# Kernel optimization log

Hardware: AMD Instinct MI355X
Metric: run time of the kernel (lower is better)

The kernel has to match this reference:

```python
import jax, jax.numpy as jnp
import numpy as np

CAPACITY_FACTOR = 1.0


def setup_inputs() -> dict:
    key = jax.random.key(0)
    ks = jax.random.split(key, 6)
    B, S, D, H, E = 4, 2048, 1024, 4096, 8
    scale_in = 1.0 / np.sqrt(D)
    scale_h = 1.0 / np.sqrt(H)
    return {
        "inputs": jax.random.normal(ks[0], (B, S, D), dtype=jnp.float32),
        "router_w": jax.random.normal(ks[1], (E, D), dtype=jnp.float32) * scale_in,
        "w1": jax.random.normal(ks[2], (E, D, H), dtype=jnp.float32) * scale_in,
        "b1": jnp.zeros((E, H), dtype=jnp.float32),
        "w2": jax.random.normal(ks[3], (E, H, D), dtype=jnp.float32) * scale_h,
        "b2": jnp.zeros((E, D), dtype=jnp.float32),
    }


def reference(inputs, router_w, w1, b1, w2, b2):
    B, S, D = inputs.shape
    E = router_w.shape[0]
    x = inputs.reshape(-1, D)                     # [T, D], T = B*S
    T = x.shape[0]
    top_k = int(CAPACITY_FACTOR * T / E)          # static: 1024

    # Router + softmax over experts (softmax_topk order), fp32 like the original
    router_logits = x @ router_w.T                # [T, E]
    all_probs = jax.nn.softmax(router_logits.astype(jnp.float32), axis=-1)

    # Expert-choice: each expert picks its top_k tokens
    weights, selected_tokens = jax.lax.top_k(all_probs.T, top_k)  # [E, K]

    # Gather tokens per expert: [E, K, D]
    xg = x[selected_tokens]

    # Per-expert MLP as grouped GEMMs (Linear -> GELU(exact) -> Linear)
    h = jax.nn.gelu(jnp.einsum("ekd,edh->ekh", xg, w1) + b1[:, None, :],
                    approximate=False)
    out = jnp.einsum("ekh,ehd->ekd", h, w2) + b2[:, None, :]   # [E, K, D]

    # Weighted scatter-add combine (indices unique within an expert;
    # cross-expert duplicates accumulate, matching the per-expert += loop)
    out = out * weights[..., None].astype(out.dtype)
    results = jnp.zeros_like(x).at[selected_tokens.reshape(-1)].add(
        out.reshape(-1, D))

    return results.reshape(B, S, D), router_logits, selected_tokens
```

## Files before the change

kernel.cpp:

```cpp
#include <hip/hip_runtime.h>
#include <hip/hip_bf16.h>
#include <math.h>

#define T_TOK 8192
#define E_EXP 8
#define D_DIM 1024
#define H_DIM 4096
#define K_CAP 1024

typedef __attribute__((ext_vector_type(8))) short short8;
typedef __attribute__((ext_vector_type(4))) float floatx4;
typedef __attribute__((ext_vector_type(16))) float floatx16;

typedef __attribute__((address_space(3))) unsigned int lds_u32_t;
typedef __attribute__((address_space(1))) unsigned int gbl_u32_t;
#define ASYNC_CP16(gptr, lptr) \
  __builtin_amdgcn_global_load_lds((gbl_u32_t*)(gptr), (lds_u32_t*)(lptr), 16, 0, 0)

static __device__ __forceinline__ unsigned int f2bf_u(float f) {
  union { float f; unsigned int u; } v; v.f = f;
  unsigned int r = v.u + 0x7FFF + ((v.u >> 16) & 1);
  return r >> 16;
}

__global__ __launch_bounds__(256) void zero_kernel(float* __restrict__ p, int n4) {
  int i = blockIdx.x * 256 + threadIdx.x;
  if (i < n4) ((floatx4*)p)[i] = (floatx4)0.0f;
}

template <int KD, int ND>
__global__ __launch_bounds__(256)
void transpose_kernel(const float* __restrict__ w, unsigned short* __restrict__ wt) {
  int e = blockIdx.z;
  int n0 = blockIdx.x * 64, k0 = blockIdx.y * 64;
  __shared__ float ts[64][65];
  int tid = threadIdx.x;
  int rr = tid >> 4;
  int cc = (tid & 15) * 4;
  const float* src = w + ((size_t)e * KD + k0 + rr) * ND + n0 + cc;
#pragma unroll
  for (int it = 0; it < 4; it++) {
    float4 v = *(const float4*)(src + (size_t)it * 16 * ND);
    int r = rr + it * 16;
    ts[r][cc + 0] = v.x; ts[r][cc + 1] = v.y; ts[r][cc + 2] = v.z; ts[r][cc + 3] = v.w;
  }
  __syncthreads();
  int n = tid >> 3;
  int k8 = (tid & 7) * 8;
#pragma unroll
  for (int it = 0; it < 2; it++) {
    int nn = n + it * 32;
    unsigned int u[4];
#pragma unroll
    for (int j = 0; j < 4; j++)
      u[j] = f2bf_u(ts[k8 + 2 * j][nn]) | (f2bf_u(ts[k8 + 2 * j + 1][nn]) << 16);
    *(uint4*)&wt[((size_t)e * ND + n0 + nn) * KD + k0 + k8] = *(uint4*)u;
  }
}

__global__ __launch_bounds__(256)
void router_kernel(const float* __restrict__ x, const float* __restrict__ rw,
                   float* __restrict__ logits_out, float* __restrict__ probs_ws,
                   unsigned long long* __restrict__ keys_ws,
                   unsigned short* __restrict__ x_bf) {
  int t = blockIdx.x;
  int tid = threadIdx.x;
  int lane = tid & 63, wid = tid >> 6;
  __shared__ float xs[D_DIM];
  __shared__ double dred[4 * E_EXP];
  __shared__ double dlog[E_EXP];
  for (int i = tid; i < D_DIM; i += 256) xs[i] = x[(size_t)t * D_DIM + i];
  __syncthreads();
  {
    int i4 = tid * 4;
    uint2 u;
    u.x = f2bf_u(xs[i4 + 0]) | (f2bf_u(xs[i4 + 1]) << 16);
    u.y = f2bf_u(xs[i4 + 2]) | (f2bf_u(xs[i4 + 3]) << 16);
    ((uint2*)(x_bf + (size_t)t * D_DIM))[tid] = u;
  }
#pragma unroll
  for (int e = 0; e < E_EXP; e++) {
    double s = 0.0;
#pragma unroll
    for (int i = 0; i < 4; i++) {
      int d = tid + i * 256;
      s += (double)xs[d] * (double)rw[e * D_DIM + d];
    }
#pragma unroll
    for (int off = 32; off > 0; off >>= 1) s += __shfl_down(s, off, 64);
    if (lane == 0) dred[wid * E_EXP + e] = s;
  }
  __syncthreads();
  if (tid < E_EXP) {
    double s = dred[tid] + dred[E_EXP + tid] + dred[2 * E_EXP + tid] + dred[3 * E_EXP + tid];
    dlog[tid] = s;
    logits_out[(size_t)t * E_EXP + tid] = (float)s;
  }
  __syncthreads();
  if (tid == 0) {
    double m = dlog[0];
#pragma unroll
    for (int e = 1; e < E_EXP; e++) m = dlog[e] > m ? dlog[e] : m;
    double ex[E_EXP], Z = 0.0;
#pragma unroll
    for (int e = 0; e < E_EXP; e++) { ex[e] = exp(dlog[e] - m); Z += ex[e]; }
#pragma unroll
    for (int e = 0; e < E_EXP; e++) {
      double p = ex[e] / Z;
      probs_ws[e * T_TOK + t] = (float)p;
      unsigned long long b = (unsigned long long)__double_as_longlong(p);
      keys_ws[e * T_TOK + t] = (b & ~8191ULL) | (unsigned long long)(8191 - t);
    }
  }
}

__global__ __launch_bounds__(256)
void topk_kernel(const unsigned long long* __restrict__ keys_ws,
                 const float* __restrict__ probs_ws,
                 int* __restrict__ sel_ws, float* __restrict__ wt_ws,
                 float* __restrict__ selout) {
  int e = blockIdx.x >> 5, seg = blockIdx.x & 31;
  int tid = threadIdx.x;
  const unsigned long long* keys = keys_ws + (size_t)e * T_TOK;
  __shared__ unsigned long long kbuf[2048];
  int t = seg * 256 + tid;
  unsigned long long own = keys[t];
  int rank = 0;
  for (int pass = 0; pass < 4; pass++) {
    __syncthreads();
    for (int j = tid; j < 2048; j += 256) kbuf[j] = keys[pass * 2048 + j];
    __syncthreads();
#pragma unroll 8
    for (int j = 0; j < 2048; j++) rank += (kbuf[j] > own);
  }
  if (rank < K_CAP) {
    sel_ws[e * K_CAP + rank] = t;
    wt_ws[e * K_CAP + rank] = probs_ws[e * T_TOK + t];
    selout[e * K_CAP + rank] = (float)t;
  }
}

template <int MODE, int KDIM, int NDIM>
__device__ __forceinline__ void gemm_core(
    int e, int m0, int n0, int kbase, int kch, bool add_bias,
    const unsigned short* __restrict__ abase,
    const unsigned short* __restrict__ bt,
    const float* __restrict__ bias,
    const int* __restrict__ sel,
    const float* __restrict__ wt,
    unsigned short* __restrict__ hout,
    float* __restrict__ results) {
  __shared__ unsigned short As[128 * 64];
  __shared__ unsigned short Bs[128 * 64];
  int tid = threadIdx.x;
  int lane = tid & 63, w = tid >> 6;
  int wave_m = w >> 1, wave_n = w & 1;

  int srow = lane >> 2;
  int scol = (lane & 3) * 8;
  int rowA0 = w * 16 + srow;
  int rowA1 = (4 + w) * 16 + srow;
  const unsigned short *arow0, *arow1;
  if (MODE == 1) {
    arow0 = abase + (size_t)sel[e * K_CAP + m0 + rowA0] * KDIM + kbase + scol;
    arow1 = abase + (size_t)sel[e * K_CAP + m0 + rowA1] * KDIM + kbase + scol;
  } else {
    arow0 = abase + ((size_t)e * K_CAP + m0 + rowA0) * KDIM + kbase + scol;
    arow1 = abase + ((size_t)e * K_CAP + m0 + rowA1) * KDIM + kbase + scol;
  }
  const unsigned short* brow0 = bt + ((size_t)e * NDIM + n0 + rowA0) * KDIM + kbase + scol;
  const unsigned short* brow1 = bt + ((size_t)e * NDIM + n0 + rowA1) * KDIM + kbase + scol;

  char* lA0 = (char*)As + w * 1024;
  char* lA1 = (char*)As + (4 + w) * 1024;
  char* lA2 = (char*)As + (8 + w) * 1024;
  char* lA3 = (char*)As + (12 + w) * 1024;
  char* lB0 = (char*)Bs + w * 1024;
  char* lB1 = (char*)Bs + (4 + w) * 1024;
  char* lB2 = (char*)Bs + (8 + w) * 1024;
  char* lB3 = (char*)Bs + (12 + w) * 1024;

  floatx16 acc[2][2];
#pragma unroll
  for (int i = 0; i < 2; i++)
#pragma unroll
    for (int j = 0; j < 2; j++) acc[i][j] = (floatx16)0.0f;

  int am = lane & 31;
  int k8 = (lane >> 5) * 8;

  for (int k0 = 0; k0 < kch; k0 += 64) {
    ASYNC_CP16(arow0, lA0);
    ASYNC_CP16(arow1, lA1);
    ASYNC_CP16(arow0 + 32, lA2);
    ASYNC_CP16(arow1 + 32, lA3);
    ASYNC_CP16(brow0, lB0);
    ASYNC_CP16(brow1, lB1);
    ASYNC_CP16(brow0 + 32, lB2);
    ASYNC_CP16(brow1 + 32, lB3);
    arow0 += 64; arow1 += 64; brow0 += 64; brow1 += 64;
    __syncthreads();
    short8 av[2][4], bv[2][4];
#pragma unroll
    for (int t = 0; t < 2; t++)
#pragma unroll
      for (int kk = 0; kk < 4; kk++) {
        int idx = (kk >> 1) * 4096 + (kk & 1) * 16 + k8;
        av[t][kk] = *(const short8*)&As[idx + (wave_m * 64 + t * 32 + am) * 32];
        bv[t][kk] = *(const short8*)&Bs[idx + (wave_n * 64 + t * 32 + am) * 32];
      }
#pragma unroll
    for (int kk = 0; kk < 4; kk++)
#pragma unroll
      for (int ti = 0; ti < 2; ti++)
#pragma unroll
        for (int tj = 0; tj < 2; tj++)
          acc[ti][tj] = __builtin_amdgcn_mfma_f32_32x32x16_bf16(
              av[ti][kk], bv[tj][kk], acc[ti][tj], 0, 0, 0);
    __syncthreads();
  }

  int hi = lane >> 5;
#pragma unroll
  for (int ti = 0; ti < 2; ti++) {
    int rbase = wave_m * 64 + ti * 32 + hi * 4;
    if (MODE == 1) {
#pragma unroll
      for (int tj = 0; tj < 2; tj++) {
        int col = n0 + wave_n * 64 + tj * 32 + am;
        float bv_ = bias[e * NDIM + col];
#pragma unroll
        for (int r = 0; r < 16; r++) {
          int m_l = rbase + (r & 3) + 8 * (r >> 2);
          float v = acc[ti][tj][r] + bv_;
          float gl = 0.5f * v * (1.0f + erff(v * 0.70710678118f));
          hout[((size_t)e * K_CAP + m0 + m_l) * H_DIM + col] = (unsigned short)f2bf_u(gl);
        }
      }
    } else {
      int toks[16]; float wgts[16];
#pragma unroll
      for (int r = 0; r < 16; r++) {
        int m_l = rbase + (r & 3) + 8 * (r >> 2);
        toks[r] = sel[e * K_CAP + m0 + m_l];
        wgts[r] = wt[e * K_CAP + m0 + m_l];
      }
#pragma unroll
      for (int tj = 0; tj < 2; tj++) {
        int col = n0 + wave_n * 64 + tj * 32 + am;
        float bv_ = add_bias ? bias[e * NDIM + col] : 0.0f;
#pragma unroll
        for (int r = 0; r < 16; r++) {
          float v = (acc[ti][tj][r] + bv_) * wgts[r];
          atomicAdd(&results[(size_t)toks[r] * D_DIM + col], v);
        }
      }
    }
  }
}

__global__ __launch_bounds__(256, 2)
void moe_gemm1(const unsigned short* __restrict__ x_bf,
               const unsigned short* __restrict__ w1t,
               const float* __restrict__ b1,
               const int* __restrict__ sel,
               unsigned short* __restrict__ h) {
  gemm_core<1, D_DIM, H_DIM>(blockIdx.z, blockIdx.y * 128, blockIdx.x * 128,
                             0, D_DIM, true, x_bf, w1t, b1, sel, nullptr, h, nullptr);
}

__global__ __launch_bounds__(256, 2)
void moe_gemm2(const unsigned short* __restrict__ h,
               const unsigned short* __restrict__ w2t,
               const float* __restrict__ b2,
               const int* __restrict__ sel,
               const float* __restrict__ wt,
               float* __restrict__ results) {
  int e = blockIdx.x;
  int rest = blockIdx.y;
  int s = rest & 1;
  int nt = (rest >> 1) & 7;
  int mt = rest >> 4;
  gemm_core<2, H_DIM, D_DIM>(e, mt * 128, nt * 128, s * (H_DIM / 2), H_DIM / 2,
                             s == 0, h, w2t, b2, sel, wt, nullptr, results);
}

extern "C" void kernel_launch(void* const* d_in, const int* in_sizes, int n_in,
                              void* d_out, int out_size, void* d_ws, size_t ws_size,
                              hipStream_t stream) {
  const float* x  = (const float*)d_in[0];
  const float* rw = (const float*)d_in[1];
  const float* w1 = (const float*)d_in[2];
  const float* b1 = (const float*)d_in[3];
  const float* w2 = (const float*)d_in[4];
  const float* b2 = (const float*)d_in[5];

  float* out_res = (float*)d_out;
  float* out_log = out_res + (size_t)T_TOK * D_DIM;
  float* out_sel = out_log + (size_t)T_TOK * E_EXP;

  char* ws = (char*)d_ws;
  float* probs_ws = (float*)ws;
  unsigned long long* keys_ws = (unsigned long long*)(ws + 262144);
  int* sel_ws = (int*)(ws + 786432);
  float* wt_ws = (float*)(ws + 819200);
  unsigned short* x_bf = (unsigned short*)(ws + 1048576);
  unsigned short* h_ws = (unsigned short*)(ws + 17825792);
  unsigned short* t_buf = (unsigned short*)(ws + 84934656);

  zero_kernel<<<(T_TOK * D_DIM / 4 + 255) / 256, 256, 0, stream>>>(out_res, T_TOK * D_DIM / 4);

  router_kernel<<<T_TOK, 256, 0, stream>>>(x, rw, out_log, probs_ws, keys_ws, x_bf);

  topk_kernel<<<256, 256, 0, stream>>>(keys_ws, probs_ws, sel_ws, wt_ws, out_sel);

  transpose_kernel<D_DIM, H_DIM><<<dim3(H_DIM / 64, D_DIM / 64, E_EXP), 256, 0, stream>>>(
      w1, t_buf);

  moe_gemm1<<<dim3(H_DIM / 128, K_CAP / 128, E_EXP), 256, 0, stream>>>(
      x_bf, t_buf, b1, sel_ws, h_ws);

  transpose_kernel<H_DIM, D_DIM><<<dim3(D_DIM / 64, H_DIM / 64, E_EXP), 256, 0, stream>>>(
      w2, t_buf);

  moe_gemm2<<<dim3(E_EXP, (D_DIM / 128) * (K_CAP / 128) * 2), 256, 0, stream>>>(
      h_ws, t_buf, b2, sel_ws, wt_ws, out_res);
}
```

Before: 681.6 us.

## Use 256x256 GEMM tiles with double-buffered swizzled LDS and 512 threads

Both grouped GEMMs move from 128x128 tiles with 4 waves to 256x256 tiles with 8 waves. Each wave now computes a 128x64 sub-tile, which raises data reuse per LDS load. The K loop double-buffers LDS (128 KB) so the async copy of the next tile overlaps the MFMAs on the current one, and it uses one barrier per iteration instead of two. An XOR swizzle on LDS addresses is meant to avoid bank conflicts. In exchange, the 128 KB of LDS per block limits occupancy to one block per CU, and gemm2 now launches only 256 blocks (gemm1 launches 512), so the grids are small relative to the CU count.

New measurement: 696.7 us. +2.2%, slower.

```diff
diff --git a/kernel.cpp b/kernel.cpp
--- a/kernel.cpp
+++ b/kernel.cpp
@@ -150,108 +150,131 @@
     const float* __restrict__ wt,
     unsigned short* __restrict__ hout,
     float* __restrict__ results) {
-  __shared__ unsigned short As[128 * 64];
-  __shared__ unsigned short Bs[128 * 64];
+  __shared__ __align__(16) unsigned char smem[131072];
   int tid = threadIdx.x;
   int lane = tid & 63, w = tid >> 6;
-  int wave_m = w >> 1, wave_n = w & 1;
-
-  int srow = lane >> 2;
-  int scol = (lane & 3) * 8;
-  int rowA0 = w * 16 + srow;
-  int rowA1 = (4 + w) * 16 + srow;
-  const unsigned short *arow0, *arow1;
-  if (MODE == 1) {
-    arow0 = abase + (size_t)sel[e * K_CAP + m0 + rowA0] * KDIM + kbase + scol;
-    arow1 = abase + (size_t)sel[e * K_CAP + m0 + rowA1] * KDIM + kbase + scol;
-  } else {
-    arow0 = abase + ((size_t)e * K_CAP + m0 + rowA0) * KDIM + kbase + scol;
-    arow1 = abase + ((size_t)e * K_CAP + m0 + rowA1) * KDIM + kbase + scol;
-  }
-  const unsigned short* brow0 = bt + ((size_t)e * NDIM + n0 + rowA0) * KDIM + kbase + scol;
-  const unsigned short* brow1 = bt + ((size_t)e * NDIM + n0 + rowA1) * KDIM + kbase + scol;
-
-  char* lA0 = (char*)As + w * 1024;
-  char* lA1 = (char*)As + (4 + w) * 1024;
-  char* lA2 = (char*)As + (8 + w) * 1024;
-  char* lA3 = (char*)As + (12 + w) * 1024;
-  char* lB0 = (char*)Bs + w * 1024;
-  char* lB1 = (char*)Bs + (4 + w) * 1024;
-  char* lB2 = (char*)Bs + (8 + w) * 1024;
-  char* lB3 = (char*)Bs + (12 + w) * 1024;
-
-  floatx16 acc[2][2];
-#pragma unroll
-  for (int i = 0; i < 2; i++)
-#pragma unroll
-    for (int j = 0; j < 2; j++) acc[i][j] = (floatx16)0.0f;
-
-  int am = lane & 31;
-  int k8 = (lane >> 5) * 8;
-
-  for (int k0 = 0; k0 < kch; k0 += 64) {
-    ASYNC_CP16(arow0, lA0);
-    ASYNC_CP16(arow1, lA1);
-    ASYNC_CP16(arow0 + 32, lA2);
-    ASYNC_CP16(arow1 + 32, lA3);
-    ASYNC_CP16(brow0, lB0);
-    ASYNC_CP16(brow1, lB1);
-    ASYNC_CP16(brow0 + 32, lB2);
-    ASYNC_CP16(brow1 + 32, lB3);
-    arow0 += 64; arow1 += 64; brow0 += 64; brow1 += 64;
+  int wm = w >> 2, wn = w & 3;
+
+  const unsigned short* srcA[4];
+  const unsigned short* srcB[4];
+  int ldsA[4], ldsB[4];
+#pragma unroll
+  for (int j = 0; j < 4; ++j) {
+    int c = j * 512 + tid;
+    int h = c >> 10;
+    int kk32 = (c >> 9) & 1;
+    int cp = c & 511;
+    int cpp = cp ^ ((cp >> 3) & 3);
+    int row = cpp >> 2, cch = cpp & 3;
+    int trow = h * 128 + row;
+    int koff = kk32 * 32 + cch * 8;
+    size_t arow;
+    if (MODE == 1) arow = (size_t)sel[e * K_CAP + m0 + trow];
+    else           arow = (size_t)e * K_CAP + m0 + trow;
+    srcA[j] = abase + arow * KDIM + kbase + koff;
+    srcB[j] = bt + ((size_t)e * NDIM + n0 + trow) * KDIM + kbase + koff;
+    ldsA[j] = c * 16;
+    ldsB[j] = 32768 + c * 16;
+  }
+
+  auto stage = [&](int b) {
+    char* Lb = (char*)smem + b * 65536;
+#pragma unroll
+    for (int j = 0; j < 4; ++j) {
+      ASYNC_CP16(srcA[j], Lb + ldsA[j]);
+      ASYNC_CP16(srcB[j], Lb + ldsB[j]);
+      srcA[j] += 64; srcB[j] += 64;
+    }
+  };
+
+  floatx16 acc[4][2];
+#pragma unroll
+  for (int i = 0; i < 4; ++i)
+#pragma unroll
+    for (int j = 0; j < 2; ++j) acc[i][j] = (floatx16)0.0f;
+
+  int rA = lane & 31;
+  int q16 = (lane >> 5) * 16;
+
+  int NT = kch / 64;
+
+  stage(0);
+  __syncthreads();
+
+  for (int kt = 0; kt < NT; ++kt) {
+    if (kt + 1 < NT) stage((kt + 1) & 1);
+
+    const char* Lb = (const char*)smem + (kt & 1) * 65536;
+    const char* Aplane = Lb + wm * 16384;
+    const char* Bplane = Lb + 32768 + (wn >> 1) * 16384;
+#pragma unroll
+    for (int half = 0; half < 2; ++half) {
+      const char* Ap = Aplane + half * 8192;
+      const char* Bp = Bplane + half * 8192;
+      short8 av[4][2], bv[2][2];
+#pragma unroll
+      for (int fm = 0; fm < 4; ++fm) {
+        int r = fm * 32 + rA;
+        int xr = ((r >> 1) & 3) << 4;
+#pragma unroll
+        for (int kk = 0; kk < 2; ++kk) {
+          int off = (r * 64 + kk * 32 + q16) ^ xr;
+          av[fm][kk] = *(const short8*)(Ap + off);
+        }
+      }
+#pragma unroll
+      for (int fn = 0; fn < 2; ++fn) {
+        int r = (wn & 1) * 64 + fn * 32 + rA;
+        int xr = ((r >> 1) & 3) << 4;
+#pragma unroll
+        for (int kk = 0; kk < 2; ++kk) {
+          int off = (r * 64 + kk * 32 + q16) ^ xr;
+          bv[fn][kk] = *(const short8*)(Bp + off);
+        }
+      }
+#pragma unroll
+      for (int kk = 0; kk < 2; ++kk)
+#pragma unroll
+        for (int fm = 0; fm < 4; ++fm)
+#pragma unroll
+          for (int fn = 0; fn < 2; ++fn)
+            acc[fm][fn] = __builtin_amdgcn_mfma_f32_32x32x16_bf16(
+                av[fm][kk], bv[fn][kk], acc[fm][fn], 0, 0, 0);
+    }
     __syncthreads();
-    short8 av[2][4], bv[2][4];
-#pragma unroll
-    for (int t = 0; t < 2; t++)
-#pragma unroll
-      for (int kk = 0; kk < 4; kk++) {
-        int idx = (kk >> 1) * 4096 + (kk & 1) * 16 + k8;
-        av[t][kk] = *(const short8*)&As[idx + (wave_m * 64 + t * 32 + am) * 32];
-        bv[t][kk] = *(const short8*)&Bs[idx + (wave_n * 64 + t * 32 + am) * 32];
-      }
-#pragma unroll
-    for (int kk = 0; kk < 4; kk++)
-#pragma unroll
-      for (int ti = 0; ti < 2; ti++)
-#pragma unroll
-        for (int tj = 0; tj < 2; tj++)
-          acc[ti][tj] = __builtin_amdgcn_mfma_f32_32x32x16_bf16(
-              av[ti][kk], bv[tj][kk], acc[ti][tj], 0, 0, 0);
-    __syncthreads();
   }
 
   int hi = lane >> 5;
 #pragma unroll
-  for (int ti = 0; ti < 2; ti++) {
-    int rbase = wave_m * 64 + ti * 32 + hi * 4;
+  for (int fm = 0; fm < 4; ++fm) {
     if (MODE == 1) {
 #pragma unroll
-      for (int tj = 0; tj < 2; tj++) {
-        int col = n0 + wave_n * 64 + tj * 32 + am;
+      for (int fn = 0; fn < 2; ++fn) {
+        int col = n0 + wn * 64 + fn * 32 + rA;
         float bv_ = bias[e * NDIM + col];
 #pragma unroll
-        for (int r = 0; r < 16; r++) {
-          int m_l = rbase + (r & 3) + 8 * (r >> 2);
-          float v = acc[ti][tj][r] + bv_;
+        for (int r = 0; r < 16; ++r) {
+          int m_l = wm * 128 + fm * 32 + (r & 3) + 8 * (r >> 2) + 4 * hi;
+          float v = acc[fm][fn][r] + bv_;
           float gl = 0.5f * v * (1.0f + erff(v * 0.70710678118f));
-          hout[((size_t)e * K_CAP + m0 + m_l) * H_DIM + col] = (unsigned short)f2bf_u(gl);
+          hout[((size_t)e * K_CAP + m0 + m_l) * NDIM + col] = (unsigned short)f2bf_u(gl);
         }
       }
     } else {
       int toks[16]; float wgts[16];
 #pragma unroll
-      for (int r = 0; r < 16; r++) {
-        int m_l = rbase + (r & 3) + 8 * (r >> 2);
+      for (int r = 0; r < 16; ++r) {
+        int m_l = wm * 128 + fm * 32 + (r & 3) + 8 * (r >> 2) + 4 * hi;
         toks[r] = sel[e * K_CAP + m0 + m_l];
         wgts[r] = wt[e * K_CAP + m0 + m_l];
       }
 #pragma unroll
-      for (int tj = 0; tj < 2; tj++) {
-        int col = n0 + wave_n * 64 + tj * 32 + am;
+      for (int fn = 0; fn < 2; ++fn) {
+        int col = n0 + wn * 64 + fn * 32 + rA;
         float bv_ = add_bias ? bias[e * NDIM + col] : 0.0f;
 #pragma unroll
-        for (int r = 0; r < 16; r++) {
-          float v = (acc[ti][tj][r] + bv_) * wgts[r];
+        for (int r = 0; r < 16; ++r) {
+          float v = (acc[fm][fn][r] + bv_) * wgts[r];
           atomicAdd(&results[(size_t)toks[r] * D_DIM + col], v);
         }
       }
@@ -259,17 +282,17 @@
   }
 }
 
-__global__ __launch_bounds__(256, 2)
+__global__ __launch_bounds__(512, 2)
 void moe_gemm1(const unsigned short* __restrict__ x_bf,
                const unsigned short* __restrict__ w1t,
                const float* __restrict__ b1,
                const int* __restrict__ sel,
                unsigned short* __restrict__ h) {
-  gemm_core<1, D_DIM, H_DIM>(blockIdx.z, blockIdx.y * 128, blockIdx.x * 128,
+  gemm_core<1, D_DIM, H_DIM>(blockIdx.z, blockIdx.y * 256, blockIdx.x * 256,
                              0, D_DIM, true, x_bf, w1t, b1, sel, nullptr, h, nullptr);
 }
 
-__global__ __launch_bounds__(256, 2)
+__global__ __launch_bounds__(512, 2)
 void moe_gemm2(const unsigned short* __restrict__ h,
                const unsigned short* __restrict__ w2t,
                const float* __restrict__ b2,
@@ -279,9 +302,9 @@
   int e = blockIdx.x;
   int rest = blockIdx.y;
   int s = rest & 1;
-  int nt = (rest >> 1) & 7;
-  int mt = rest >> 4;
-  gemm_core<2, H_DIM, D_DIM>(e, mt * 128, nt * 128, s * (H_DIM / 2), H_DIM / 2,
+  int nt = (rest >> 1) & 3;
+  int mt = rest >> 3;
+  gemm_core<2, H_DIM, D_DIM>(e, mt * 256, nt * 256, s * (H_DIM / 2), H_DIM / 2,
                              s == 0, h, w2t, b2, sel, wt, nullptr, results);
 }
 
@@ -317,12 +340,12 @@
   transpose_kernel<D_DIM, H_DIM><<<dim3(H_DIM / 64, D_DIM / 64, E_EXP), 256, 0, stream>>>(
       w1, t_buf);
 
-  moe_gemm1<<<dim3(H_DIM / 128, K_CAP / 128, E_EXP), 256, 0, stream>>>(
+  moe_gemm1<<<dim3(H_DIM / 256, K_CAP / 256, E_EXP), 512, 0, stream>>>(
       x_bf, t_buf, b1, sel_ws, h_ws);
 
   transpose_kernel<H_DIM, D_DIM><<<dim3(D_DIM / 64, H_DIM / 64, E_EXP), 256, 0, stream>>>(
       w2, t_buf);
 
-  moe_gemm2<<<dim3(E_EXP, (D_DIM / 128) * (K_CAP / 128) * 2), 256, 0, stream>>>(
+  moe_gemm2<<<dim3(E_EXP, 32), 512, 0, stream>>>(
       h_ws, t_buf, b2, sel_ws, wt_ws, out_res);
 }
```
